# Kernel tuning notes

Measured on AMD Instinct MI355X. Metric: run time of the kernel, lower is better.

Reference implementation:

```python
import jax, jax.numpy as jnp
import numpy as np
from jax.scipy.special import erf, digamma, i0

B, L, D, H = 4, 4096, 512, 4
_MAX_SQRT_GRADIENT = 1000.0

@jax.custom_vjp
def sqrt_bound(x):
    return jnp.sqrt(x)

def _sb_fwd(x):
    return jnp.sqrt(x), x

def _sb_bwd(x, g):
    return (g / jnp.sqrt(jnp.clip(4.0 * x, 1.0 / _MAX_SQRT_GRADIENT**2, None)),)

sqrt_bound.defvjp(_sb_fwd, _sb_bwd)

def block_diag_linear(x, w):
    # x: [..., D], w: [h, bw, bw] block-diagonal weight
    h, bw, _ = w.shape
    xr = x.reshape(x.shape[:-1] + (h, bw))
    return jnp.einsum('...hi,hij->...hj', xr, w).reshape(x.shape)

def self_att_pool(x, num_heads):
    n_state = x.shape[-1] // num_heads
    attn = jax.nn.softmax(jnp.einsum('bld,bmd->blm', x, x) / np.float32(np.sqrt(n_state)), axis=-1)
    # max over the sequence axis of the attended values, keepdims -> [B,1,D]
    return jnp.max(jnp.einsum('blm,bmd->bld', attn, x), axis=-2, keepdims=True)

def ripple_transform_hybrid(t, mix_params):
    mix = jax.nn.softmax(mix_params)
    return mix[0] * digamma(t + 1.0) + mix[1] * i0(t)

def ripple_act(data, alpha, beta, mix_params, temperature=1.0):
    def f(d):
        norm = erf(d / (jnp.max(d) * alpha))
        return jnp.sum(ripple_transform_hybrid(norm * beta, mix_params))
    g = jnp.clip(jax.grad(f)(data), -1.0, 1.0)
    return jax.nn.softmax(-g / temperature, axis=-1)  # softmin

def ripplemoe_act(data, weights, alphas, beta, mix_params, temperature=1.0):
    def f(d):
        dmax = jnp.max(d)
        norm = erf(d[None] / (dmax * alphas[:, None, None]))  # [S,B,L]
        t = ripple_transform_hybrid(norm * beta, mix_params)
        w = jax.nn.softmax(weights)
        return jnp.sum(w[:, None, None] * t)
    g = jnp.clip(jax.grad(f)(data), -1.0, 1.0)
    return jax.nn.softmax(-g / temperature, axis=-1)  # softmin

def token_selection(x, cls_w, cls_b, token_weights, prelu_a, ts_weights, ts_alphas, ts_beta, ts_mix):
    scores = jnp.einsum('bld,sd->sbl', x, cls_w) + cls_b[:, None, None]  # [S,B,L]
    p = jnp.where(scores >= 0, scores, prelu_a * scores)  # PReLU
    ts = jax.nn.celu(p) * jax.nn.silu(p) + jax.nn.gelu(p, approximate=False)
    combined = jnp.einsum('s,sbl->bl', jax.nn.selu(token_weights[:, 0]), ts)
    _, idx = jax.lax.top_k(combined, combined.shape[-1])  # k = L, descending permutation
    vals = ts.sum(0)  # [B,L]
    b_idx = jnp.arange(combined.shape[0])[:, None]
    importance = jnp.ones_like(combined).at[b_idx, idx].add(vals)
    return (1.0 + ripplemoe_act(importance, ts_weights, ts_alphas, ts_beta, ts_mix))[..., None]

def _forward(x, attention_space, W_spatial, W_sil, W_ohead, W_out, w_ig, w_ag, a_param,
             cls_w, cls_b, token_weights, prelu_a, ts_weights, ts_alphas, ts_beta, ts_mix,
             pa1_alpha, pa1_beta, pa1_mix, pa2_alpha, pa2_beta, pa2_mix):
    spatial = jnp.einsum('bld,de->ble', x, attention_space) @ W_spatial.T
    # RG-LRU style gating
    gate_x = jax.nn.sigmoid(block_diag_linear(x, w_ig))
    gate_a = jax.nn.sigmoid(block_diag_linear(x, w_ag))
    log_a = -8.0 * jax.nn.softplus(a_param) * gate_a
    normalized_x = x * gate_x * sqrt_bound(1.0 - jnp.exp(2.0 * log_a))
    gated = jnp.exp(log_a) * self_att_pool(spatial, H) + normalized_x
    sparsity = ripple_act(gated @ W_sil.T, pa1_alpha, pa1_beta, pa1_mix)
    attn = (gated * sparsity) @ W_ohead.T
    sel = token_selection(x, cls_w, cls_b, token_weights, prelu_a, ts_weights, ts_alphas, ts_beta, ts_mix)
    out = ripple_act(attn * sel, pa2_alpha, pa2_beta, pa2_mix)
    return out @ W_out.T

def setup_inputs() -> dict:
    key = jax.random.key(0)
    ks = jax.random.split(key, 12)
    lim = float(1.0 / np.sqrt(D))
    xav = float(np.sqrt(6.0 / (2 * D)))
    bw = D // H
    u = jax.random.uniform(ks[8], (D,), jnp.float32, 0.9**2 + 1e-8, 0.999**2 + 1e-8)
    return {
        'x': jax.random.normal(ks[0], (B, L, D), jnp.float32),
        'attention_space': jax.random.uniform(ks[1], (D, D), jnp.float32, -xav, xav),
        'W_spatial': jax.random.uniform(ks[2], (D, D), jnp.float32, -lim, lim),
        'W_sil': jax.random.uniform(ks[3], (D, D), jnp.float32, -lim, lim),
        'W_ohead': jax.random.uniform(ks[4], (D, D), jnp.float32, -lim, lim),
        'W_out': jax.random.uniform(ks[5], (D, D), jnp.float32, -lim, lim),
        'w_ig': jax.random.normal(ks[6], (H, bw, bw), jnp.float32) * np.float32(np.sqrt(1.0 / bw)),
        'w_ag': jax.random.normal(ks[7], (H, bw, bw), jnp.float32) * np.float32(np.sqrt(1.0 / bw)),
        'a_param': jnp.log(jnp.exp(-0.5 * jnp.log(u)) - 1.0),
        'cls_w': jax.random.uniform(ks[9], (H, D), jnp.float32, -lim, lim),
        'cls_b': jax.random.uniform(ks[10], (H,), jnp.float32, -lim, lim),
        'token_weights': jax.random.normal(ks[11], (H, 1), jnp.float32),
        'prelu_a': jnp.array(0.25, jnp.float32),
        'ts_weights': jnp.ones(H, jnp.float32) / H,
        'ts_alphas': jnp.ones(H, jnp.float32),
        'ts_beta': jnp.array(1.0, jnp.float32),
        'ts_mix': jnp.full((2,), 0.5, jnp.float32),
        'pa1_alpha': jnp.array(1.0, jnp.float32),
        'pa1_beta': jnp.array(1.0, jnp.float32),
        'pa1_mix': jnp.full((2,), 0.5, jnp.float32),
        'pa2_alpha': jnp.array(1.0, jnp.float32),
        'pa2_beta': jnp.array(1.0, jnp.float32),
        'pa2_mix': jnp.full((2,), 0.5, jnp.float32),
    }

def reference(x, attention_space, W_spatial, W_sil, W_ohead, W_out, w_ig, w_ag, a_param,
              cls_w, cls_b, token_weights, prelu_a, ts_weights, ts_alphas, ts_beta, ts_mix,
              pa1_alpha, pa1_beta, pa1_mix, pa2_alpha, pa2_beta, pa2_mix):
    return _forward(x, attention_space, W_spatial, W_sil, W_ohead, W_out, w_ig, w_ag, a_param,
                    cls_w, cls_b, token_weights, prelu_a, ts_weights, ts_alphas, ts_beta, ts_mix,
                    pa1_alpha, pa1_beta, pa1_mix, pa2_alpha, pa2_beta, pa2_mix)
```

## Files before the change

kernel.cpp:

```cpp
#include <hip/hip_runtime.h>

typedef unsigned short ushort;
typedef unsigned int uint;
typedef unsigned long long u64;

#define DEV __device__ __forceinline__

typedef __attribute__((ext_vector_type(4))) float f32x4;
typedef __bf16 bf16x8 __attribute__((ext_vector_type(8)));
typedef __attribute__((ext_vector_type(4))) ushort u16x4;
typedef __attribute__((ext_vector_type(8))) ushort u16x8;

static constexpr int B_ = 4, L_ = 4096, D_ = 512;
static constexpr long NE = (long)B_ * L_ * D_;

DEV float b2f(ushort u) { return __uint_as_float(((uint)u) << 16); }
DEV ushort f2b(float f) {
    uint u = __float_as_uint(f);
    uint r = u + 0x7FFFu + ((u >> 16) & 1u);
    return (ushort)(r >> 16);
}
DEV uint mapF(float f) {
    uint b = __float_as_uint(f);
    return (b & 0x80000000u) ? ~b : (b | 0x80000000u);
}
DEV float unmapF(uint u) {
    uint b = (u & 0x80000000u) ? (u & 0x7FFFFFFFu) : ~u;
    return __uint_as_float(b);
}
DEV float rcp_(float x) { return __builtin_amdgcn_rcpf(x); }
DEV float fexp(float x) { return __builtin_amdgcn_exp2f(x * 1.44269504089f); }
DEV float sigm(float x) { return rcp_(1.f + fexp(-x)); }

DEV void gload16(const ushort* g, ushort* l) {
    __builtin_amdgcn_global_load_lds((const __attribute__((address_space(1))) void*)g,
                                     (__attribute__((address_space(3))) void*)l, 16, 0, 0);
}

DEV int xcd_swz(int b, int nwg) {
    int q = nwg >> 3, r = nwg & 7;
    int x = b & 7, i = b >> 3;
    int base = (x < r) ? x * (q + 1) : r * (q + 1) + (x - r) * q;
    return base + i;
}

DEV float trigamma1p(float t) {
    float x = t + 1.f;
    float acc = 0.f;
#pragma unroll
    for (int k = 0; k < 6; k++) { float xx = x + (float)k; acc += rcp_(xx * xx); }
    float y = x + 6.f;
    float iy = rcp_(y), iy2 = iy * iy;
    return acc + iy * (1.f + iy * (0.5f + iy * (0.166666667f + iy2 * (-0.0333333333f + iy2 * 0.0238095238f))));
}
DEV float besselI1(float t) {
    float q = 0.25f * t * t;
    return 0.5f * t * (1.f + q * (0.5f + q * (0.0833333333f + q * (0.00694444444f + q * (3.47222222e-4f + q * 1.15740741e-5f)))));
}
DEV float rippleH(float u, float beta, float mix0, float mix1) {
    float t = beta * erff(u);
    float Tp = mix0 * trigamma1p(t) + mix1 * besselI1(t);
    float ep = 1.12837917f * fexp(-u * u);
    return beta * Tp * ep;
}

DEV void gemm_core(const ushort* __restrict__ A, int lda,
                   const ushort* __restrict__ Bt, int ldb, int K,
                   ushort* __restrict__ Alds, ushort* __restrict__ Blds,
                   f32x4 (&acc)[4][4])
{
    const int tid = threadIdx.x;
    const int lane = tid & 63;
    const int wave = tid >> 6;
    const int wr = wave >> 1, wc = wave & 1;

    const int srow = wave * 16 + (lane >> 2);
    const int skc = (lane & 3) * 8;
    const ushort* Ag0 = A + (size_t)srow * lda + skc;
    const ushort* Ag1 = A + (size_t)(srow + 64) * lda + skc;
    const ushort* Bg0 = Bt + (size_t)srow * ldb + skc;
    const ushort* Bg1 = Bt + (size_t)(srow + 64) * ldb + skc;
    const int wb = wave * 512;

    const int ar = wr * 64 + (lane & 15);
    const int br = wc * 64 + (lane & 15);
    const int kk = (lane >> 4) * 8;

    gload16(Ag0, Alds + wb);
    gload16(Ag1, Alds + 2048 + wb);
    gload16(Bg0, Blds + wb);
    gload16(Bg1, Blds + 2048 + wb);
    __syncthreads();

    int cur = 0;
    for (int k0 = 0; k0 < K; k0 += 32) {
        const int nb = cur ^ 1;
        if (k0 + 32 < K) {
            gload16(Ag0 + k0 + 32, Alds + nb * 4096 + wb);
            gload16(Ag1 + k0 + 32, Alds + nb * 4096 + 2048 + wb);
            gload16(Bg0 + k0 + 32, Blds + nb * 4096 + wb);
            gload16(Bg1 + k0 + 32, Blds + nb * 4096 + 2048 + wb);
        }
        bf16x8 af[4], bfr[4];
#pragma unroll
        for (int mi = 0; mi < 4; mi++) af[mi] = *(const bf16x8*)&Alds[cur * 4096 + (ar + mi * 16) * 32 + kk];
#pragma unroll
        for (int ni = 0; ni < 4; ni++) bfr[ni] = *(const bf16x8*)&Blds[cur * 4096 + (br + ni * 16) * 32 + kk];
#pragma unroll
        for (int mi = 0; mi < 4; mi++)
#pragma unroll
            for (int ni = 0; ni < 4; ni++)
                acc[mi][ni] = __builtin_amdgcn_mfma_f32_16x16x32_bf16(af[mi], bfr[ni], acc[mi][ni], 0, 0, 0);
        __syncthreads();
        cur = nb;
    }
}

template <int MODE, bool DOMAX>
__global__ __launch_bounds__(256, 2) void gemm_bt(
    const ushort* __restrict__ A, int lda,
    const ushort* __restrict__ Bt, int ldb,
    void* __restrict__ Cv, int ldc, int K,
    const float* __restrict__ rowScale, u64* __restrict__ pmax)
{
    __shared__ ushort Alds[2 * 128 * 32];
    __shared__ ushort Blds[2 * 128 * 32];
    const int nwg = gridDim.x * gridDim.y;
    const int s = xcd_swz(blockIdx.y * gridDim.x + blockIdx.x, nwg);
    const int bx = s % gridDim.x, by = s / gridDim.x;
    const int row0 = by * 128, col0 = bx * 128;
    f32x4 acc[4][4] = {};
    gemm_core(A + (size_t)row0 * lda, lda, Bt + (size_t)col0 * ldb, ldb, K, Alds, Blds, acc);

    const int tid = threadIdx.x;
    const int lane = tid & 63;
    const int wave = tid >> 6;
    const int wr = wave >> 1, wc = wave & 1;
    const int ocol = col0 + wc * 64 + (lane & 15);
    u64 lp = 0;
#pragma unroll
    for (int mi = 0; mi < 4; mi++) {
        const int rbase = row0 + wr * 64 + mi * 16 + (lane >> 4) * 4;
#pragma unroll
        for (int j = 0; j < 4; j++) {
            float sc = (MODE == 3) ? rowScale[rbase + j] : 1.f;
#pragma unroll
            for (int ni = 0; ni < 4; ni++) {
                float v = acc[mi][ni][j] * sc;
                int cc = ocol + ni * 16;
                if (MODE == 1) ((ushort*)Cv)[(size_t)(rbase + j) * ldc + cc] = f2b(v);
                else ((float*)Cv)[(size_t)(rbase + j) * ldc + cc] = v;
                if (DOMAX) {
                    uint idx = (uint)((rbase + j) * ldc + cc);
                    u64 p = ((u64)mapF(v) << 32) | (u64)(~idx);
                    lp = (p > lp) ? p : lp;
                }
            }
        }
    }
    if (DOMAX) {
#pragma unroll
        for (int off = 32; off > 0; off >>= 1) {
            u64 o = __shfl_xor(lp, off);
            lp = (o > lp) ? o : lp;
        }
        if (lane == 0) atomicMax(pmax, lp);
    }
}

__global__ __launch_bounds__(256, 2) void pv_split_k(const ushort* __restrict__ P, const ushort* __restrict__ Vt,
                                                     float* __restrict__ part)
{
    __shared__ ushort Alds[2 * 128 * 32];
    __shared__ ushort Blds[2 * 128 * 32];
    const int ks = blockIdx.z;
    const int nwg = gridDim.x * gridDim.y;
    const int s = xcd_swz(blockIdx.y * gridDim.x + blockIdx.x, nwg);
    const int bx = s % gridDim.x, by = s / gridDim.x;
    const int row0 = by * 128, col0 = bx * 128;
    f32x4 acc[4][4] = {};
    gemm_core(P + (size_t)row0 * 4096 + ks * 1024, 4096,
              Vt + (size_t)col0 * 4096 + ks * 1024, 4096, 1024, Alds, Blds, acc);

    float* C = part + (size_t)ks * 2097152 + (size_t)row0 * 512 + col0;
    const int tid = threadIdx.x;
    const int lane = tid & 63;
    const int wave = tid >> 6;
    const int wr = wave >> 1, wc = wave & 1;
    const int ocol = wc * 64 + (lane & 15);
#pragma unroll
    for (int mi = 0; mi < 4; mi++) {
        const int rl = wr * 64 + mi * 16 + (lane >> 4) * 4;
#pragma unroll
        for (int j = 0; j < 4; j++)
#pragma unroll
            for (int ni = 0; ni < 4; ni++)
                C[(size_t)(rl + j) * 512 + ocol + ni * 16] = acc[mi][ni][j];
    }
}

__global__ __launch_bounds__(256) void pool_combine_k(const float* __restrict__ part, uint* __restrict__ poolU)
{
    const int tid = threadIdx.x;
    const int l0 = blockIdx.x * 32;
    float m0 = -3.4e38f, m1 = -3.4e38f;
    for (int l = 0; l < 32; l++) {
        size_t off = (size_t)(l0 + l) * 512;
        float s0 = 0.f, s1 = 0.f;
#pragma unroll
        for (int ks = 0; ks < 4; ks++) {
            s0 += part[(size_t)ks * 2097152 + off + tid];
            s1 += part[(size_t)ks * 2097152 + off + tid + 256];
        }
        m0 = fmaxf(m0, s0); m1 = fmaxf(m1, s1);
    }
    atomicMax(&poolU[tid], mapF(m0));
    atomicMax(&poolU[tid + 256], mapF(m1));
}

__global__ __launch_bounds__(256, 2) void gate_gemm_k(const ushort* __restrict__ xb,
                                                      const ushort* __restrict__ wigT, const ushort* __restrict__ wagT,
                                                      ushort* __restrict__ gxab, ushort* __restrict__ gaab)
{
    __shared__ ushort Alds[2 * 128 * 32];
    __shared__ ushort Blds[2 * 128 * 32];
    const int which = blockIdx.x;
    const int h = blockIdx.z;
    const ushort* A = xb + (size_t)blockIdx.y * 128 * 512 + h * 128;
    const ushort* W = (which ? wagT : wigT) + (size_t)h * 16384;
    f32x4 acc[4][4] = {};
    gemm_core(A, 512, W, 128, 128, Alds, Blds, acc);

    ushort* C = (which ? gaab : gxab) + (size_t)blockIdx.y * 128 * 512 + h * 128;
    const int tid = threadIdx.x;
    const int lane = tid & 63;
    const int wave = tid >> 6;
    const int wr = wave >> 1, wc = wave & 1;
    const int ocol = wc * 64 + (lane & 15);
#pragma unroll
    for (int mi = 0; mi < 4; mi++) {
        const int rl = wr * 64 + mi * 16 + (lane >> 4) * 4;
#pragma unroll
        for (int j = 0; j < 4; j++)
#pragma unroll
            for (int ni = 0; ni < 4; ni++)
                C[(size_t)(rl + j) * 512 + ocol + ni * 16] = f2b(acc[mi][ni][j]);
    }
}

__global__ void convert_f2b_k(const float* __restrict__ s, ushort* __restrict__ d, long n4) {
    long i = (long)blockIdx.x * blockDim.x + threadIdx.x;
    long st = (long)gridDim.x * blockDim.x;
    for (; i < n4; i += st) {
        f32x4 v = ((const f32x4*)s)[i];
        u16x4 o;
        o[0] = f2b(v[0]); o[1] = f2b(v[1]); o[2] = f2b(v[2]); o[3] = f2b(v[3]);
        ((u16x4*)d)[i] = o;
    }
}

__global__ void convert_w4_k(const float* __restrict__ w0, const float* __restrict__ w1,
                             const float* __restrict__ w2, const float* __restrict__ w3,
                             ushort* __restrict__ dst) {
    const float* srcs[4] = {w0, w1, w2, w3};
    const float* s = srcs[blockIdx.y];
    ushort* d = dst + (size_t)blockIdx.y * 262144;
    int i = blockIdx.x * 256 + threadIdx.x;
    f32x4 v = ((const f32x4*)s)[i];
    u16x4 o;
    o[0] = f2b(v[0]); o[1] = f2b(v[1]); o[2] = f2b(v[2]); o[3] = f2b(v[3]);
    ((u16x4*)d)[i] = o;
}

template <bool SRCF32>
__global__ __launch_bounds__(256) void transpose_to_bf16(const void* __restrict__ srcv, ushort* __restrict__ dst, int R, int C) {
    __shared__ float tile[32][33];
    const int z = blockIdx.z;
    const float* sf = (const float*)srcv + (size_t)z * R * C;
    const ushort* sb = (const ushort*)srcv + (size_t)z * R * C;
    ushort* dz = dst + (size_t)z * R * C;
    const int tx = threadIdx.x & 31, ty = threadIdx.x >> 5;
    const int c = blockIdx.x * 32 + tx;
#pragma unroll
    for (int k = 0; k < 4; k++) {
        const int r = blockIdx.y * 32 + ty + k * 8;
        tile[ty + k * 8][tx] = SRCF32 ? sf[(size_t)r * C + c] : b2f(sb[(size_t)r * C + c]);
    }
    __syncthreads();
#pragma unroll
    for (int k = 0; k < 4; k++) {
        const int dr = blockIdx.x * 32 + ty + k * 8;
        const int dc = blockIdx.y * 32 + tx;
        dz[(size_t)dr * R + dc] = f2b(tile[tx][ty + k * 8]);
    }
}

__global__ __launch_bounds__(256) void transpose_gates_k(const float* __restrict__ wig, const float* __restrict__ wag,
                                                         ushort* __restrict__ wigT, ushort* __restrict__ wagT) {
    __shared__ float tile[32][33];
    const int which = blockIdx.z >> 2, h = blockIdx.z & 3;
    const float* src = (which ? wag : wig) + (size_t)h * 16384;
    ushort* dst = (which ? wagT : wigT) + (size_t)h * 16384;
    const int tx = threadIdx.x & 31, ty = threadIdx.x >> 5;
    const int c = blockIdx.x * 32 + tx;
#pragma unroll
    for (int k = 0; k < 4; k++) {
        const int r = blockIdx.y * 32 + ty + k * 8;
        tile[ty + k * 8][tx] = src[(size_t)r * 128 + c];
    }
    __syncthreads();
#pragma unroll
    for (int k = 0; k < 4; k++) {
        const int dr = blockIdx.x * 32 + ty + k * 8;
        const int dc = blockIdx.y * 32 + tx;
        dst[(size_t)dr * 128 + dc] = f2b(tile[tx][ty + k * 8]);
    }
}

__global__ void init_misc_k(uint* poolU, u64* pmax) {
    int i = blockIdx.x * 256 + threadIdx.x;
    if (i < 2048) poolU[i] = 0u;
    if (i < 4) pmax[i] = 0ull;
}
__global__ void sentinel_k(float* o) { o[threadIdx.x] = 1.0e6f; }

__global__ __launch_bounds__(256) void gates_gated_k(const float* __restrict__ x, const ushort* __restrict__ gxab,
                                                     const ushort* __restrict__ gaab, const float* __restrict__ a_param,
                                                     const uint* __restrict__ poolU, ushort* __restrict__ gatedb) {
    __shared__ float sp8[512];
    const int tid = threadIdx.x;
    for (int d = tid; d < 512; d += 256) {
        float a = a_param[d];
        sp8[d] = 8.f * (fmaxf(a, 0.f) + log1pf(expf(-fabsf(a))));
    }
    __syncthreads();
    long i = (long)blockIdx.x * blockDim.x + tid;
    long st = (long)gridDim.x * blockDim.x;
    const long n8 = NE >> 3;
    for (; i < n8; i += st) {
        u16x8 gx8 = ((const u16x8*)gxab)[i];
        u16x8 ga8 = ((const u16x8*)gaab)[i];
        f32x4 x0 = ((const f32x4*)x)[2 * i];
        f32x4 x1 = ((const f32x4*)x)[2 * i + 1];
        long e = i << 3;
        int b = (int)(e >> 21);
        int d0 = (int)(e & 511);
        u16x8 o;
#pragma unroll
        for (int j = 0; j < 8; j++) {
            float xv = (j < 4) ? x0[j] : x1[j - 4];
            float gx = sigm(b2f(gx8[j]));
            float ga = sigm(b2f(ga8[j]));
            float la = -sp8[d0 + j] * ga;
            float ea = fexp(la);
            float nx = xv * gx * sqrtf(fmaxf(1.f - fexp(2.f * la), 0.f));
            float pl = unmapF(poolU[b * 512 + d0 + j]);
            o[j] = f2b(ea * pl + nx);
        }
        ((u16x8*)gatedb)[i] = o;
    }
}

__global__ __launch_bounds__(256) void softmax_rows_k(const ushort* __restrict__ S, ushort* __restrict__ P, float scale) {
    __shared__ float red[256];
    const int tid = threadIdx.x;
    const ushort* row = S + (size_t)blockIdx.x * 4096;
    float vals[16];
    bf16x8 v0 = *(const bf16x8*)&row[tid * 16];
    bf16x8 v1 = *(const bf16x8*)&row[tid * 16 + 8];
    float mx = -3.4e38f;
#pragma unroll
    for (int k = 0; k < 8; k++) { vals[k] = (float)v0[k] * scale; mx = fmaxf(mx, vals[k]); }
#pragma unroll
    for (int k = 0; k < 8; k++) { vals[8 + k] = (float)v1[k] * scale; mx = fmaxf(mx, vals[8 + k]); }
    red[tid] = mx; __syncthreads();
    for (int s = 128; s > 0; s >>= 1) { if (tid < s) red[tid] = fmaxf(red[tid], red[tid + s]); __syncthreads(); }
    mx = red[0]; __syncthreads();
    float sum = 0.f;
#pragma unroll
    for (int k = 0; k < 16; k++) { vals[k] = fexp(vals[k] - mx); sum += vals[k]; }
    red[tid] = sum; __syncthreads();
    for (int s = 128; s > 0; s >>= 1) { if (tid < s) red[tid] += red[tid + s]; __syncthreads(); }
    float inv = rcp_(red[0]);
    ushort* prow = P + (size_t)blockIdx.x * 4096;
#pragma unroll
    for (int k = 0; k < 16; k++) prow[tid * 16 + k] = f2b(vals[k] * inv);
}

__global__ __launch_bounds__(256) void redmax1_k(const float* __restrict__ d, long n, float* __restrict__ bmax, int* __restrict__ bidx) {
    __shared__ float rv[256];
    __shared__ int ri[256];
    const int tid = threadIdx.x;
    long g = (long)blockIdx.x * 256 + tid;
    const long stride = (long)gridDim.x * 256;
    float bv = -3.4e38f; int bi = -1;
    for (long i = g; i < n; i += stride) {
        float v = d[i];
        if (v > bv) { bv = v; bi = (int)i; }
    }
    rv[tid] = bv; ri[tid] = bi; __syncthreads();
    for (int s = 128; s > 0; s >>= 1) {
        if (tid < s) {
            float ov = rv[tid + s]; int oi = ri[tid + s];
            if (oi >= 0 && (ri[tid] < 0 || ov > rv[tid] || (ov == rv[tid] && oi < ri[tid]))) { rv[tid] = ov; ri[tid] = oi; }
        }
        __syncthreads();
    }
    if (tid == 0) { bmax[blockIdx.x] = rv[0]; bidx[blockIdx.x] = ri[0]; }
}
__global__ __launch_bounds__(256) void redmax2_k(const float* __restrict__ bmax, const int* __restrict__ bidx, int n,
                                                 float* __restrict__ outM, int* __restrict__ outI) {
    __shared__ float rv[256];
    __shared__ int ri[256];
    const int tid = threadIdx.x;
    float bv = -3.4e38f; int bi = -1;
    for (int i = tid; i < n; i += 256) {
        float v = bmax[i]; int ix = bidx[i];
        if (ix >= 0 && (bi < 0 || v > bv || (v == bv && ix < bi))) { bv = v; bi = ix; }
    }
    rv[tid] = bv; ri[tid] = bi; __syncthreads();
    for (int s = 128; s > 0; s >>= 1) {
        if (tid < s) {
            float ov = rv[tid + s]; int oi = ri[tid + s];
            if (oi >= 0 && (ri[tid] < 0 || ov > rv[tid] || (ov == rv[tid] && oi < ri[tid]))) { rv[tid] = ov; ri[tid] = oi; }
        }
        __syncthreads();
    }
    if (tid == 0) { outM[0] = rv[0]; outI[0] = ri[0]; }
}

__global__ __launch_bounds__(256) void ripple_g_k(const float* __restrict__ d, float* __restrict__ gb, float* __restrict__ sspart,
                                                  const u64* __restrict__ pmax, const float* __restrict__ alpha_p,
                                                  const float* __restrict__ beta_p, const float* __restrict__ mix_p) {
    __shared__ float red[256];
    const int tid = threadIdx.x;
    const float M = unmapF((uint)(pmax[0] >> 32));
    const float alpha = alpha_p[0], beta = beta_p[0];
    float m0 = mix_p[0], m1 = mix_p[1];
    float mm = fmaxf(m0, m1);
    float e0 = fexp(m0 - mm), e1 = fexp(m1 - mm);
    float inv = rcp_(e0 + e1);
    float mix0 = e0 * inv, mix1 = e1 * inv;
    const float invMA = rcp_(M * alpha);
    float ss = 0.f;
    long g = (long)blockIdx.x * 256 + tid;
    const long stride = (long)gridDim.x * 256;
    for (long i = g; i < NE; i += stride) {
        float dv = d[i];
        float H = rippleH(dv * invMA, beta, mix0, mix1);
        gb[i] = H * invMA;
        ss += H * dv;
    }
    red[tid] = ss; __syncthreads();
    for (int s = 128; s > 0; s >>= 1) { if (tid < s) red[tid] += red[tid + s]; __syncthreads(); }
    if (tid == 0) sspart[blockIdx.x] = red[0];
}
__global__ __launch_bounds__(256) void redsum2_k(const float* __restrict__ part, int n, float* __restrict__ out) {
    __shared__ float red[256];
    const int tid = threadIdx.x;
    float s = 0.f;
    for (int i = tid; i < n; i += 256) s += part[i];
    red[tid] = s; __syncthreads();
    for (int q = 128; q > 0; q >>= 1) { if (tid < q) red[tid] += red[tid + q]; __syncthreads(); }
    if (tid == 0) out[0] = red[0];
}

template <int GS>
__global__ __launch_bounds__(256) void ripple_softmax_k(const float* __restrict__ gb,
                                                        const u64* __restrict__ pmax,
                                                        const float* __restrict__ ssTot, const float* __restrict__ alpha_p,
                                                        const ushort* __restrict__ gatedb, ushort* __restrict__ outb) {
    __shared__ float red[256];
    const int tid = threadIdx.x;
    const float M = unmapF((uint)(pmax[0] >> 32));
    const int amax = (int)(~(uint)(pmax[0] & 0xFFFFFFFFull));
    const float corr = ssTot[0] * rcp_(M * M * alpha_p[0]);
    long base = (long)blockIdx.x * 512;
    float g0 = gb[base + tid];
    float g1 = gb[base + tid + 256];
    if ((int)(base + tid) == amax) g0 -= corr;
    if ((int)(base + tid + 256) == amax) g1 -= corr;
    g0 = fminf(fmaxf(g0, -1.f), 1.f);
    g1 = fminf(fmaxf(g1, -1.f), 1.f);
    float mn = fminf(g0, g1);
    red[tid] = mn; __syncthreads();
    for (int s = 128; s > 0; s >>= 1) { if (tid < s) red[tid] = fminf(red[tid], red[tid + s]); __syncthreads(); }
    mn = red[0]; __syncthreads();
    float e0 = fexp(mn - g0), e1 = fexp(mn - g1);
    red[tid] = e0 + e1; __syncthreads();
    for (int s = 128; s > 0; s >>= 1) { if (tid < s) red[tid] += red[tid + s]; __syncthreads(); }
    float inv = rcp_(red[0]);
    if (GS) {
        outb[base + tid] = f2b(b2f(gatedb[base + tid]) * (e0 * inv));
        outb[base + tid + 256] = f2b(b2f(gatedb[base + tid + 256]) * (e1 * inv));
    } else {
        outb[base + tid] = f2b(e0 * inv);
        outb[base + tid + 256] = f2b(e1 * inv);
    }
}

__global__ __launch_bounds__(256) void ts1_k(const float* __restrict__ x, const float* __restrict__ cls_w,
                                             const float* __restrict__ cls_b, const float* __restrict__ tw,
                                             const float* __restrict__ prelu_a,
                                             float* __restrict__ combined, float* __restrict__ vals) {
    __shared__ float cw[2048];
    const int tid = threadIdx.x;
    for (int i = tid; i < 2048; i += 256) cw[i] = cls_w[i];
    __syncthreads();
    const int lane = tid & 63, wid = tid >> 6;
    const int row = blockIdx.x * 4 + wid;
    const float* xr = x + (size_t)row * 512 + lane * 8;
    float pa0 = 0, pa1 = 0, pa2 = 0, pa3 = 0;
#pragma unroll
    for (int j = 0; j < 8; j++) {
        float v = xr[j];
        int c = lane * 8 + j;
        pa0 += v * cw[c]; pa1 += v * cw[512 + c]; pa2 += v * cw[1024 + c]; pa3 += v * cw[1536 + c];
    }
#pragma unroll
    for (int o = 32; o > 0; o >>= 1) {
        pa0 += __shfl_down(pa0, o); pa1 += __shfl_down(pa1, o);
        pa2 += __shfl_down(pa2, o); pa3 += __shfl_down(pa3, o);
    }
    if (lane == 0) {
        float a = prelu_a[0];
        float sc[4] = {pa0, pa1, pa2, pa3};
        float comb = 0.f, vsum = 0.f;
#pragma unroll
        for (int s = 0; s < 4; s++) {
            float p = sc[s] + cls_b[s];
            p = (p >= 0.f) ? p : a * p;
            float cel = (p > 0.f) ? p : expm1f(p);
            float sil = p * sigm(p);
            float gel = 0.5f * p * (1.f + erff(p * 0.70710678f));
            float ts = cel * sil + gel;
            float ww = tw[s];
            float se = 1.05070099f * ((ww > 0.f) ? ww : 1.67326324f * expm1f(ww));
            comb += se * ts;
            vsum += ts;
        }
        combined[row] = comb;
        vals[row] = vsum;
    }
}

__global__ __launch_bounds__(256) void ts2a_k(const float* __restrict__ combined, int* __restrict__ rankp) {
    __shared__ float q[512];
    const int b = blockIdx.z;
    const int tid = threadIdx.x;
    const float* cr = combined + b * 4096;
    const int q0 = blockIdx.y * 512;
    for (int i = tid; i < 512; i += 256) q[i] = cr[q0 + i];
    __syncthreads();
    const int p = blockIdx.x * 256 + tid;
    const float cp = cr[p];
    const f32x4* q4 = (const f32x4*)q;
    int rank = 0;
#pragma unroll 8
    for (int i4 = 0; i4 < 128; i4++) {
        f32x4 v = q4[i4];
        int qb = q0 + i4 * 4;
        rank += (v[0] > cp) || (v[0] == cp && (qb + 0) < p);
        rank += (v[1] > cp) || (v[1] == cp && (qb + 1) < p);
        rank += (v[2] > cp) || (v[2] == cp && (qb + 2) < p);
        rank += (v[3] > cp) || (v[3] == cp && (qb + 3) < p);
    }
    rankp[((b * 8 + blockIdx.y) * 4096) + p] = rank;
}

__global__ __launch_bounds__(256) void ts2b_k(const int* __restrict__ rankp, const float* __restrict__ vals,
                                              float* __restrict__ imp) {
    const int b = blockIdx.y;
    const int p = blockIdx.x * 256 + threadIdx.x;
    int rank = 0;
#pragma unroll
    for (int c = 0; c < 8; c++) rank += rankp[((b * 8 + c) * 4096) + p];
    imp[b * 4096 + p] = 1.f + vals[b * 4096 + rank];
}

__global__ __launch_bounds__(256) void moe_g_k(const float* __restrict__ imp, float* __restrict__ gmoe,
                                               float* __restrict__ sspart, const float* __restrict__ scalM,
                                               const float* __restrict__ tsw, const float* __restrict__ tsa,
                                               const float* __restrict__ tsb, const float* __restrict__ tsmix) {
    __shared__ float red[256];
    const int tid = threadIdx.x;
    const float M = scalM[0];
    float w[4], invMA[4], invA[4];
    {
        float wm = fmaxf(fmaxf(tsw[0], tsw[1]), fmaxf(tsw[2], tsw[3]));
        float s = 0.f;
#pragma unroll
        for (int k = 0; k < 4; k++) { w[k] = fexp(tsw[k] - wm); s += w[k]; }
        float si = rcp_(s);
#pragma unroll
        for (int k = 0; k < 4; k++) { w[k] *= si; invMA[k] = rcp_(M * tsa[k]); invA[k] = rcp_(tsa[k]); }
    }
    const float beta = tsb[0];
    float m0 = tsmix[0], m1 = tsmix[1];
    float mm = fmaxf(m0, m1);
    float e0 = fexp(m0 - mm), e1 = fexp(m1 - mm);
    float minv = rcp_(e0 + e1);
    const float mix0 = e0 * minv, mix1 = e1 * minv;

    float ss = 0.f;
    int i = blockIdx.x * 256 + tid;
    const int stride = gridDim.x * 256;
    for (; i < 65536; i += stride) {
        float dv = imp[i];
        float gbv = 0.f;
#pragma unroll
        for (int s = 0; s < 4; s++) {
            float H = rippleH(dv * invMA[s], beta, mix0, mix1);
            gbv += w[s] * H * invMA[s];
            ss += w[s] * H * dv * invA[s];
        }
        gmoe[i] = gbv;
    }
    red[tid] = ss; __syncthreads();
    for (int s = 128; s > 0; s >>= 1) { if (tid < s) red[tid] += red[tid + s]; __syncthreads(); }
    if (tid == 0) sspart[blockIdx.x] = red[0];
}

__global__ __launch_bounds__(256) void moe_sel_k(const float* __restrict__ gmoe, const float* __restrict__ scalM,
                                                 const int* __restrict__ scalI, const float* __restrict__ ssTot,
                                                 float* __restrict__ sel) {
    __shared__ float red[256];
    const int tid = threadIdx.x;
    const int b = blockIdx.x;
    const float M = scalM[0];
    const int amax = scalI[0];
    const float corr = ssTot[0] * rcp_(M * M);
    float g[16];
    float mn = 3.4e38f;
#pragma unroll
    for (int k = 0; k < 16; k++) {
        int i = b * 4096 + tid + k * 256;
        float v = gmoe[i];
        if (i == amax) v -= corr;
        v = fminf(fmaxf(v, -1.f), 1.f);
        g[k] = v;
        mn = fminf(mn, v);
    }
    red[tid] = mn; __syncthreads();
    for (int s = 128; s > 0; s >>= 1) { if (tid < s) red[tid] = fminf(red[tid], red[tid + s]); __syncthreads(); }
    mn = red[0]; __syncthreads();
    float sum = 0.f;
#pragma unroll
    for (int k = 0; k < 16; k++) { g[k] = fexp(mn - g[k]); sum += g[k]; }
    red[tid] = sum; __syncthreads();
    for (int s = 128; s > 0; s >>= 1) { if (tid < s) red[tid] += red[tid + s]; __syncthreads(); }
    float inv = rcp_(red[0]);
#pragma unroll
    for (int k = 0; k < 16; k++) sel[b * 4096 + tid + k * 256] = 1.f + g[k] * inv;
}

static constexpr size_t OFF_XB    = 0;
static constexpr size_t OFF_TMPB  = 16777216;
static constexpr size_t OFF_SPB   = 33554432;
static constexpr size_t OFF_SPT   = 50331648;
static constexpr size_t OFF_DBUF  = 67108864;
static constexpr size_t OFF_HBUF  = 100663296;
static constexpr size_t OFF_GATB  = 134217728;
static constexpr size_t OFF_NXB   = 150994944;
static constexpr size_t OFF_EAB   = 167772160;
static constexpr size_t OFF_AST   = 184549376;
static constexpr size_t OFF_WSP   = 185073664;
static constexpr size_t OFF_WSIL  = 185597952;
static constexpr size_t OFF_WOH   = 186122240;
static constexpr size_t OFF_WOUT  = 186646528;
static constexpr size_t OFF_WIGT  = 187170816;
static constexpr size_t OFF_WAGT  = 187301888;
static constexpr size_t OFF_POOL  = 187432960;
static constexpr size_t OFF_SCAL  = 187441152;
static constexpr size_t OFF_SCALI = 187441408;
static constexpr size_t OFF_BMAX  = 187441664;
static constexpr size_t OFF_BIDX  = 187449856;
static constexpr size_t OFF_SSP   = 187458048;
static constexpr size_t OFF_COMB  = 187466240;
static constexpr size_t OFF_VALS  = 187728384;
static constexpr size_t OFF_IMP   = 187990528;
static constexpr size_t OFF_GMOE  = 188252672;
static constexpr size_t OFF_SEL   = 188514816;
static constexpr size_t WS_NEED   = 188776960;

extern "C" void kernel_launch(void* const* d_in, const int* in_sizes, int n_in,
                              void* d_out, int out_size, void* d_ws, size_t ws_size,
                              hipStream_t stream)
{
    (void)in_sizes; (void)n_in; (void)out_size;
    const float* x    = (const float*)d_in[0];
    const float* AS   = (const float*)d_in[1];
    const float* Wsp  = (const float*)d_in[2];
    const float* Wsil = (const float*)d_in[3];
    const float* Woh  = (const float*)d_in[4];
    const float* Wout = (const float*)d_in[5];
    const float* wig  = (const float*)d_in[6];
    const float* wag  = (const float*)d_in[7];
    const float* a_param = (const float*)d_in[8];
    const float* cls_w = (const float*)d_in[9];
    const float* cls_b = (const float*)d_in[10];
    const float* tokw  = (const float*)d_in[11];
    const float* prelu = (const float*)d_in[12];
    const float* tsw   = (const float*)d_in[13];
    const float* tsa   = (const float*)d_in[14];
    const float* tsb   = (const float*)d_in[15];
    const float* tsmix = (const float*)d_in[16];
    const float* p1a = (const float*)d_in[17];
    const float* p1b = (const float*)d_in[18];
    const float* p1m = (const float*)d_in[19];
    const float* p2a = (const float*)d_in[20];
    const float* p2b = (const float*)d_in[21];
    const float* p2m = (const float*)d_in[22];
    float* out = (float*)d_out;

    char* w = (char*)d_ws;
    if (ws_size < WS_NEED) { sentinel_k<<<1, 256, 0, stream>>>(out); return; }

    ushort* xb    = (ushort*)(w + OFF_XB);
    ushort* tmpb  = (ushort*)(w + OFF_TMPB);
    ushort* spb   = (ushort*)(w + OFF_SPB);
    ushort* spT   = (ushort*)(w + OFF_SPT);
    float*  dbuf  = (float*)(w + OFF_DBUF);
    float*  Hbuf  = (float*)(w + OFF_HBUF);
    ushort* Sb    = (ushort*)(w + OFF_DBUF);
    ushort* Pb    = (ushort*)(w + OFF_HBUF);
    float*  pvpart= (float*)(w + OFF_XB);
    int*    rankp = (int*)(w + OFF_DBUF);
    ushort* gatedb= (ushort*)(w + OFF_GATB);
    ushort* gxab  = (ushort*)(w + OFF_NXB);
    ushort* gaab  = (ushort*)(w + OFF_EAB);
    ushort* ASt   = (ushort*)(w + OFF_AST);
    ushort* Wspb  = (ushort*)(w + OFF_WSP);
    ushort* Wsilb = (ushort*)(w + OFF_WSIL);
    ushort* Wohb  = (ushort*)(w + OFF_WOH);
    ushort* Woutb = (ushort*)(w + OFF_WOUT);
    ushort* wigT  = (ushort*)(w + OFF_WIGT);
    ushort* wagT  = (ushort*)(w + OFF_WAGT);
    uint*   poolU = (uint*)(w + OFF_POOL);
    float*  scal  = (float*)(w + OFF_SCAL);
    u64*    pmax  = (u64*)(w + OFF_SCAL + 128);
    int*    scalI = (int*)(w + OFF_SCALI);
    float*  bmax  = (float*)(w + OFF_BMAX);
    int*    bidx  = (int*)(w + OFF_BIDX);
    float*  sspart= (float*)(w + OFF_SSP);
    float*  comb  = (float*)(w + OFF_COMB);
    float*  vals  = (float*)(w + OFF_VALS);
    float*  imp   = (float*)(w + OFF_IMP);
    float*  gmoe  = (float*)(w + OFF_GMOE);
    float*  sel   = (float*)(w + OFF_SEL);
    ushort* gsb     = tmpb;
    ushort* probs2b = xb;

    convert_f2b_k<<<2048, 256, 0, stream>>>(x, xb, NE >> 2);
    convert_w4_k<<<dim3(256, 4), 256, 0, stream>>>(Wsp, Wsil, Woh, Wout, Wspb);
    transpose_to_bf16<true><<<dim3(16, 16, 1), 256, 0, stream>>>(AS, ASt, 512, 512);
    transpose_gates_k<<<dim3(4, 4, 8), 256, 0, stream>>>(wig, wag, wigT, wagT);
    init_misc_k<<<8, 256, 0, stream>>>(poolU, pmax);

    gate_gemm_k<<<dim3(2, 128, 4), 256, 0, stream>>>(xb, wigT, wagT, gxab, gaab);

    gemm_bt<1, false><<<dim3(4, 128), 256, 0, stream>>>(xb, 512, ASt, 512, tmpb, 512, 512, nullptr, nullptr);
    gemm_bt<1, false><<<dim3(4, 128), 256, 0, stream>>>(tmpb, 512, Wspb, 512, spb, 512, 512, nullptr, nullptr);

    transpose_to_bf16<false><<<dim3(16, 128, 4), 256, 0, stream>>>(spb, spT, 4096, 512);
    const float sc128 = 0.0883883476f;
    for (int b = 0; b < 4; b++) {
        const ushort* spB = spb + (size_t)b * L_ * D_;
        gemm_bt<1, false><<<dim3(32, 32), 256, 0, stream>>>(spB, 512, spB, 512, Sb, 4096, 512, nullptr, nullptr);
        softmax_rows_k<<<4096, 256, 0, stream>>>(Sb, Pb, sc128);
        pv_split_k<<<dim3(4, 32, 4), 256, 0, stream>>>(Pb, spT + (size_t)b * D_ * L_, pvpart);
        pool_combine_k<<<128, 256, 0, stream>>>(pvpart, poolU + b * 512);
    }

    gates_gated_k<<<1024, 256, 0, stream>>>(x, gxab, gaab, a_param, poolU, gatedb);

    gemm_bt<0, true><<<dim3(4, 128), 256, 0, stream>>>(gatedb, 512, Wsilb, 512, dbuf, 512, 512, nullptr, &pmax[0]);
    ripple_g_k<<<2048, 256, 0, stream>>>(dbuf, Hbuf, sspart, &pmax[0], p1a, p1b, p1m);
    redsum2_k<<<1, 256, 0, stream>>>(sspart, 2048, &scal[1]);
    ripple_softmax_k<1><<<16384, 256, 0, stream>>>(Hbuf, &pmax[0], &scal[1], p1a, gatedb, gsb);

    ts1_k<<<4096, 256, 0, stream>>>(x, cls_w, cls_b, tokw, prelu, comb, vals);
    ts2a_k<<<dim3(16, 8, 4), 256, 0, stream>>>(comb, rankp);
    ts2b_k<<<dim3(16, 4), 256, 0, stream>>>(rankp, vals, imp);
    redmax1_k<<<64, 256, 0, stream>>>(imp, 65536, bmax, bidx);
    redmax2_k<<<1, 256, 0, stream>>>(bmax, bidx, 64, &scal[4], &scalI[2]);
    moe_g_k<<<64, 256, 0, stream>>>(imp, gmoe, sspart, &scal[4], tsw, tsa, tsb, tsmix);
    redsum2_k<<<1, 256, 0, stream>>>(sspart, 64, &scal[5]);
    moe_sel_k<<<4, 256, 0, stream>>>(gmoe, &scal[4], &scalI[2], &scal[5], sel);

    gemm_bt<3, true><<<dim3(4, 128), 256, 0, stream>>>(gsb, 512, Wohb, 512, dbuf, 512, 512, sel, &pmax[1]);

    ripple_g_k<<<2048, 256, 0, stream>>>(dbuf, Hbuf, sspart, &pmax[1], p2a, p2b, p2m);
    redsum2_k<<<1, 256, 0, stream>>>(sspart, 2048, &scal[3]);
    ripple_softmax_k<0><<<16384, 256, 0, stream>>>(Hbuf, &pmax[1], &scal[3], p2a, nullptr, probs2b);

    gemm_bt<0, false><<<dim3(4, 128), 256, 0, stream>>>(probs2b, 512, Woutb, 512, out, 512, 512, nullptr, nullptr);
}
```

Baseline: 648.1 us.

## Fuse softmax exponentiation into PV GEMM and defer row normalization

The softmax kernel now writes only the per-row max and reciprocal sum, and the PV GEMM loads raw bf16 scores, exponentiates them in registers and stores the probabilities into LDS itself. Normalization moves into pool_combine as a per-row scale. This removes the write and re-read of the full 4096x4096 bf16 probability matrix per batch. Split-K drops from 4 to 2 and launch bounds rise to 4 waves per SIMD on the GEMMs, which trades register budget for occupancy. The A operand now takes a register-staged load path instead of the direct global-to-LDS load, and the exp work runs inside the main loop.

After: 706.5 us. 1.09x slower.

```diff
diff --git a/kernel.cpp b/kernel.cpp
--- a/kernel.cpp
+++ b/kernel.cpp
@@ -117,7 +117,7 @@
 }
 
 template <int MODE, bool DOMAX>
-__global__ __launch_bounds__(256, 2) void gemm_bt(
+__global__ __launch_bounds__(256, 4) void gemm_bt(
     const ushort* __restrict__ A, int lda,
     const ushort* __restrict__ Bt, int ldb,
     void* __restrict__ Cv, int ldc, int K,
@@ -168,8 +168,8 @@
     }
 }
 
-__global__ __launch_bounds__(256, 2) void pv_split_k(const ushort* __restrict__ P, const ushort* __restrict__ Vt,
-                                                     float* __restrict__ part)
+__global__ __launch_bounds__(256, 4) void pv_fused_k(const ushort* __restrict__ S, const ushort* __restrict__ Vt,
+                                                     const float* __restrict__ mrow, float* __restrict__ part)
 {
     __shared__ ushort Alds[2 * 128 * 32];
     __shared__ ushort Blds[2 * 128 * 32];
@@ -178,15 +178,83 @@
     const int s = xcd_swz(blockIdx.y * gridDim.x + blockIdx.x, nwg);
     const int bx = s % gridDim.x, by = s / gridDim.x;
     const int row0 = by * 128, col0 = bx * 128;
-    f32x4 acc[4][4] = {};
-    gemm_core(P + (size_t)row0 * 4096 + ks * 1024, 4096,
-              Vt + (size_t)col0 * 4096 + ks * 1024, 4096, 1024, Alds, Blds, acc);
-
-    float* C = part + (size_t)ks * 2097152 + (size_t)row0 * 512 + col0;
+    const int koff = ks * 2048;
+    const float sc128 = 0.0883883476f;
+
     const int tid = threadIdx.x;
     const int lane = tid & 63;
     const int wave = tid >> 6;
     const int wr = wave >> 1, wc = wave & 1;
+    const int srow = wave * 16 + (lane >> 2);
+    const int skc = (lane & 3) * 8;
+    const float mr0 = mrow[row0 + srow];
+    const float mr1 = mrow[row0 + srow + 64];
+    const ushort* Ag0 = S + (size_t)(row0 + srow) * 4096 + koff + skc;
+    const ushort* Ag1 = S + (size_t)(row0 + srow + 64) * 4096 + koff + skc;
+    const ushort* Bg0 = Vt + (size_t)(col0 + srow) * 4096 + koff + skc;
+    const ushort* Bg1 = Vt + (size_t)(col0 + srow + 64) * 4096 + koff + skc;
+    const int wb = wave * 512;
+    const int aoff0 = srow * 32 + skc;
+    const int aoff1 = (srow + 64) * 32 + skc;
+
+    const int ar = wr * 64 + (lane & 15);
+    const int br = wc * 64 + (lane & 15);
+    const int kk = (lane >> 4) * 8;
+
+    f32x4 acc[4][4] = {};
+
+    {
+        u16x8 a0 = *(const u16x8*)Ag0;
+        u16x8 a1 = *(const u16x8*)Ag1;
+        gload16(Bg0, Blds + wb);
+        gload16(Bg1, Blds + 2048 + wb);
+        u16x8 p0, p1;
+#pragma unroll
+        for (int j = 0; j < 8; j++) {
+            p0[j] = f2b(fexp(b2f(a0[j]) * sc128 - mr0));
+            p1[j] = f2b(fexp(b2f(a1[j]) * sc128 - mr1));
+        }
+        *(u16x8*)&Alds[aoff0] = p0;
+        *(u16x8*)&Alds[aoff1] = p1;
+    }
+    __syncthreads();
+
+    int cur = 0;
+    for (int k0 = 0; k0 < 2048; k0 += 32) {
+        const int nb = cur ^ 1;
+        const bool more = (k0 + 32) < 2048;
+        u16x8 na0, na1;
+        if (more) {
+            na0 = *(const u16x8*)(Ag0 + k0 + 32);
+            na1 = *(const u16x8*)(Ag1 + k0 + 32);
+            gload16(Bg0 + k0 + 32, Blds + nb * 4096 + wb);
+            gload16(Bg1 + k0 + 32, Blds + nb * 4096 + 2048 + wb);
+        }
+        bf16x8 af[4], bfr[4];
+#pragma unroll
+        for (int mi = 0; mi < 4; mi++) af[mi] = *(const bf16x8*)&Alds[cur * 4096 + (ar + mi * 16) * 32 + kk];
+#pragma unroll
+        for (int ni = 0; ni < 4; ni++) bfr[ni] = *(const bf16x8*)&Blds[cur * 4096 + (br + ni * 16) * 32 + kk];
+#pragma unroll
+        for (int mi = 0; mi < 4; mi++)
+#pragma unroll
+            for (int ni = 0; ni < 4; ni++)
+                acc[mi][ni] = __builtin_amdgcn_mfma_f32_16x16x32_bf16(af[mi], bfr[ni], acc[mi][ni], 0, 0, 0);
+        if (more) {
+            u16x8 p0, p1;
+#pragma unroll
+            for (int j = 0; j < 8; j++) {
+                p0[j] = f2b(fexp(b2f(na0[j]) * sc128 - mr0));
+                p1[j] = f2b(fexp(b2f(na1[j]) * sc128 - mr1));
+            }
+            *(u16x8*)&Alds[nb * 4096 + aoff0] = p0;
+            *(u16x8*)&Alds[nb * 4096 + aoff1] = p1;
+        }
+        __syncthreads();
+        cur = nb;
+    }
+
+    float* C = part + (size_t)ks * 2097152 + (size_t)row0 * 512 + col0;
     const int ocol = wc * 64 + (lane & 15);
 #pragma unroll
     for (int mi = 0; mi < 4; mi++) {
@@ -199,26 +267,24 @@
     }
 }
 
-__global__ __launch_bounds__(256) void pool_combine_k(const float* __restrict__ part, uint* __restrict__ poolU)
+__global__ __launch_bounds__(256) void pool_combine_k(const float* __restrict__ part, const float* __restrict__ invs,
+                                                      uint* __restrict__ poolU)
 {
     const int tid = threadIdx.x;
     const int l0 = blockIdx.x * 32;
     float m0 = -3.4e38f, m1 = -3.4e38f;
     for (int l = 0; l < 32; l++) {
         size_t off = (size_t)(l0 + l) * 512;
-        float s0 = 0.f, s1 = 0.f;
-#pragma unroll
-        for (int ks = 0; ks < 4; ks++) {
-            s0 += part[(size_t)ks * 2097152 + off + tid];
-            s1 += part[(size_t)ks * 2097152 + off + tid + 256];
-        }
+        float iv = invs[l0 + l];
+        float s0 = (part[off + tid] + part[2097152 + off + tid]) * iv;
+        float s1 = (part[off + tid + 256] + part[2097152 + off + tid + 256]) * iv;
         m0 = fmaxf(m0, s0); m1 = fmaxf(m1, s1);
     }
     atomicMax(&poolU[tid], mapF(m0));
     atomicMax(&poolU[tid + 256], mapF(m1));
 }
 
-__global__ __launch_bounds__(256, 2) void gate_gemm_k(const ushort* __restrict__ xb,
+__global__ __launch_bounds__(256, 4) void gate_gemm_k(const ushort* __restrict__ xb,
                                                       const ushort* __restrict__ wigT, const ushort* __restrict__ wagT,
                                                       ushort* __restrict__ gxab, ushort* __restrict__ gaab)
 {
@@ -361,7 +427,8 @@
     }
 }
 
-__global__ __launch_bounds__(256) void softmax_rows_k(const ushort* __restrict__ S, ushort* __restrict__ P, float scale) {
+__global__ __launch_bounds__(256) void softmax_stats_k(const ushort* __restrict__ S, float* __restrict__ mrow,
+                                                       float* __restrict__ invs, float scale) {
     __shared__ float red[256];
     const int tid = threadIdx.x;
     const ushort* row = S + (size_t)blockIdx.x * 4096;
@@ -378,13 +445,10 @@
     mx = red[0]; __syncthreads();
     float sum = 0.f;
 #pragma unroll
-    for (int k = 0; k < 16; k++) { vals[k] = fexp(vals[k] - mx); sum += vals[k]; }
+    for (int k = 0; k < 16; k++) sum += fexp(vals[k] - mx);
     red[tid] = sum; __syncthreads();
     for (int s = 128; s > 0; s >>= 1) { if (tid < s) red[tid] += red[tid + s]; __syncthreads(); }
-    float inv = rcp_(red[0]);
-    ushort* prow = P + (size_t)blockIdx.x * 4096;
-#pragma unroll
-    for (int k = 0; k < 16; k++) prow[tid * 16 + k] = f2b(vals[k] * inv);
+    if (tid == 0) { mrow[blockIdx.x] = mx; invs[blockIdx.x] = rcp_(red[0]); }
 }
 
 __global__ __launch_bounds__(256) void redmax1_k(const float* __restrict__ d, long n, float* __restrict__ bmax, int* __restrict__ bidx) {
@@ -723,7 +787,8 @@
     float*  dbuf  = (float*)(w + OFF_DBUF);
     float*  Hbuf  = (float*)(w + OFF_HBUF);
     ushort* Sb    = (ushort*)(w + OFF_DBUF);
-    ushort* Pb    = (ushort*)(w + OFF_HBUF);
+    float*  mrow  = (float*)(w + OFF_HBUF);
+    float*  invs  = (float*)(w + OFF_HBUF) + 4096;
     float*  pvpart= (float*)(w + OFF_XB);
     int*    rankp = (int*)(w + OFF_DBUF);
     ushort* gatedb= (ushort*)(w + OFF_GATB);
@@ -767,9 +832,9 @@
     for (int b = 0; b < 4; b++) {
         const ushort* spB = spb + (size_t)b * L_ * D_;
         gemm_bt<1, false><<<dim3(32, 32), 256, 0, stream>>>(spB, 512, spB, 512, Sb, 4096, 512, nullptr, nullptr);
-        softmax_rows_k<<<4096, 256, 0, stream>>>(Sb, Pb, sc128);
-        pv_split_k<<<dim3(4, 32, 4), 256, 0, stream>>>(Pb, spT + (size_t)b * D_ * L_, pvpart);
-        pool_combine_k<<<128, 256, 0, stream>>>(pvpart, poolU + b * 512);
+        softmax_stats_k<<<4096, 256, 0, stream>>>(Sb, mrow, invs, sc128);
+        pv_fused_k<<<dim3(4, 32, 2), 256, 0, stream>>>(Sb, spT + (size_t)b * D_ * L_, mrow, pvpart);
+        pool_combine_k<<<128, 256, 0, stream>>>(pvpart, invs, poolU + b * 512);
     }
 
     gates_gated_k<<<1024, 256, 0, stream>>>(x, gxab, gaab, a_param, poolU, gatedb);
```

## Exploit symmetry of x·xᵀ with 256-tile triangular GEMM, batch pairs, in-place softmax

Applied to the files above, without the earlier changes.

Replaces the per-batch 128x128 S=sp·spᵀ GEMM with a 256x256-tile kernel that computes only upper-triangle tiles and writes each off-diagonal tile plus its transpose, processing two batches per launch. The row softmax now runs in place over both batches with vectorized stores. Launch bounds on the other GEMMs are raised to 4 waves per SIMD. This roughly halves the MFMA work and kernel count for the attention scores, at the cost of strided transposed stores and more register pressure in the 512-thread kernel.

Measured after the change: 657.4 us. No clear change (+1.4%).

```diff
diff --git a/kernel.cpp b/kernel.cpp
--- a/kernel.cpp
+++ b/kernel.cpp
@@ -117,7 +117,7 @@
 }
 
 template <int MODE, bool DOMAX>
-__global__ __launch_bounds__(256, 2) void gemm_bt(
+__global__ __launch_bounds__(256, 4) void gemm_bt(
     const ushort* __restrict__ A, int lda,
     const ushort* __restrict__ Bt, int ldb,
     void* __restrict__ Cv, int ldc, int K,
@@ -168,7 +168,97 @@
     }
 }
 
-__global__ __launch_bounds__(256, 2) void pv_split_k(const ushort* __restrict__ P, const ushort* __restrict__ Vt,
+__global__ __launch_bounds__(512, 1) void gemm256_sym_k(
+    const ushort* __restrict__ spP,
+    ushort* __restrict__ Sout)
+{
+    __shared__ ushort Alds[2 * 256 * 32];
+    __shared__ ushort Blds[2 * 256 * 32];
+    const int z = blockIdx.z;
+    int t = xcd_swz(blockIdx.x, 136);
+    int by = 0;
+    while (t >= 16 - by) { t -= 16 - by; by++; }
+    const int bx = by + t;
+    const int row0 = by * 256, col0 = bx * 256;
+    const ushort* A = spP + (size_t)z * (4096 * 512) + (size_t)row0 * 512;
+    const ushort* Bt = spP + (size_t)z * (4096 * 512) + (size_t)col0 * 512;
+
+    const int tid = threadIdx.x;
+    const int lane = tid & 63;
+    const int wave = tid >> 6;
+    const int wr = wave >> 2, wc = wave & 3;
+
+    const int srow = wave * 32 + (lane >> 2);
+    const int skc = (lane & 3) * 8;
+    const ushort* Ag0 = A + (size_t)srow * 512 + skc;
+    const ushort* Ag1 = A + (size_t)(srow + 16) * 512 + skc;
+    const ushort* Bg0 = Bt + (size_t)srow * 512 + skc;
+    const ushort* Bg1 = Bt + (size_t)(srow + 16) * 512 + skc;
+    const int wb = wave * 1024;
+
+    const int ar = wr * 128 + (lane & 15);
+    const int br = wc * 64 + (lane & 15);
+    const int kk = (lane >> 4) * 8;
+
+    f32x4 acc[8][4] = {};
+
+    gload16(Ag0, Alds + wb);
+    gload16(Ag1, Alds + wb + 512);
+    gload16(Bg0, Blds + wb);
+    gload16(Bg1, Blds + wb + 512);
+    __syncthreads();
+
+    int cur = 0;
+    for (int k0 = 0; k0 < 512; k0 += 32) {
+        const int nb = cur ^ 1;
+        if (k0 + 32 < 512) {
+            gload16(Ag0 + k0 + 32, Alds + nb * 8192 + wb);
+            gload16(Ag1 + k0 + 32, Alds + nb * 8192 + wb + 512);
+            gload16(Bg0 + k0 + 32, Blds + nb * 8192 + wb);
+            gload16(Bg1 + k0 + 32, Blds + nb * 8192 + wb + 512);
+        }
+        bf16x8 af[8], bfr[4];
+#pragma unroll
+        for (int mi = 0; mi < 8; mi++) af[mi] = *(const bf16x8*)&Alds[cur * 8192 + (ar + mi * 16) * 32 + kk];
+#pragma unroll
+        for (int ni = 0; ni < 4; ni++) bfr[ni] = *(const bf16x8*)&Blds[cur * 8192 + (br + ni * 16) * 32 + kk];
+#pragma unroll
+        for (int mi = 0; mi < 8; mi++)
+#pragma unroll
+            for (int ni = 0; ni < 4; ni++)
+                acc[mi][ni] = __builtin_amdgcn_mfma_f32_16x16x32_bf16(af[mi], bfr[ni], acc[mi][ni], 0, 0, 0);
+        __syncthreads();
+        cur = nb;
+    }
+
+    ushort* C = Sout + (size_t)z * 16777216;
+    const int ocol = col0 + wc * 64 + (lane & 15);
+#pragma unroll
+    for (int mi = 0; mi < 8; mi++) {
+        const int rbase = row0 + wr * 128 + mi * 16 + (lane >> 4) * 4;
+#pragma unroll
+        for (int j = 0; j < 4; j++)
+#pragma unroll
+            for (int ni = 0; ni < 4; ni++)
+                C[(size_t)(rbase + j) * 4096 + ocol + ni * 16] = f2b(acc[mi][ni][j]);
+    }
+    if (by != bx) {
+#pragma unroll
+        for (int ni = 0; ni < 4; ni++) {
+            const int c = ocol + ni * 16;
+#pragma unroll
+            for (int mi = 0; mi < 8; mi++) {
+                const int r0 = row0 + wr * 128 + mi * 16 + (lane >> 4) * 4;
+                u16x4 v;
+#pragma unroll
+                for (int j = 0; j < 4; j++) v[j] = f2b(acc[mi][ni][j]);
+                *(u16x4*)&C[(size_t)c * 4096 + r0] = v;
+            }
+        }
+    }
+}
+
+__global__ __launch_bounds__(256, 4) void pv_split_k(const ushort* __restrict__ P, const ushort* __restrict__ Vt,
                                                      float* __restrict__ part)
 {
     __shared__ ushort Alds[2 * 128 * 32];
@@ -218,7 +308,7 @@
     atomicMax(&poolU[tid + 256], mapF(m1));
 }
 
-__global__ __launch_bounds__(256, 2) void gate_gemm_k(const ushort* __restrict__ xb,
+__global__ __launch_bounds__(256, 4) void gate_gemm_k(const ushort* __restrict__ xb,
                                                       const ushort* __restrict__ wigT, const ushort* __restrict__ wagT,
                                                       ushort* __restrict__ gxab, ushort* __restrict__ gaab)
 {
@@ -361,10 +451,11 @@
     }
 }
 
-__global__ __launch_bounds__(256) void softmax_rows_k(const ushort* __restrict__ S, ushort* __restrict__ P, float scale) {
+__global__ __launch_bounds__(256) void softmax_rows_k(ushort* __restrict__ Sbase, float scale) {
     __shared__ float red[256];
     const int tid = threadIdx.x;
-    const ushort* row = S + (size_t)blockIdx.x * 4096;
+    const int r = blockIdx.x;
+    ushort* row = Sbase + (size_t)(r >> 12) * 16777216 + (size_t)(r & 4095) * 4096;
     float vals[16];
     bf16x8 v0 = *(const bf16x8*)&row[tid * 16];
     bf16x8 v1 = *(const bf16x8*)&row[tid * 16 + 8];
@@ -382,9 +473,11 @@
     red[tid] = sum; __syncthreads();
     for (int s = 128; s > 0; s >>= 1) { if (tid < s) red[tid] += red[tid + s]; __syncthreads(); }
     float inv = rcp_(red[0]);
-    ushort* prow = P + (size_t)blockIdx.x * 4096;
-#pragma unroll
-    for (int k = 0; k < 16; k++) prow[tid * 16 + k] = f2b(vals[k] * inv);
+    u16x8 o0, o1;
+#pragma unroll
+    for (int k = 0; k < 8; k++) { o0[k] = f2b(vals[k] * inv); o1[k] = f2b(vals[8 + k] * inv); }
+    *(u16x8*)&row[tid * 16] = o0;
+    *(u16x8*)&row[tid * 16 + 8] = o1;
 }
 
 __global__ __launch_bounds__(256) void redmax1_k(const float* __restrict__ d, long n, float* __restrict__ bmax, int* __restrict__ bidx) {
@@ -722,8 +815,7 @@
     ushort* spT   = (ushort*)(w + OFF_SPT);
     float*  dbuf  = (float*)(w + OFF_DBUF);
     float*  Hbuf  = (float*)(w + OFF_HBUF);
-    ushort* Sb    = (ushort*)(w + OFF_DBUF);
-    ushort* Pb    = (ushort*)(w + OFF_HBUF);
+    ushort* Spair = (ushort*)(w + OFF_DBUF);
     float*  pvpart= (float*)(w + OFF_XB);
     int*    rankp = (int*)(w + OFF_DBUF);
     ushort* gatedb= (ushort*)(w + OFF_GATB);
@@ -764,12 +856,16 @@
 
     transpose_to_bf16<false><<<dim3(16, 128, 4), 256, 0, stream>>>(spb, spT, 4096, 512);
     const float sc128 = 0.0883883476f;
-    for (int b = 0; b < 4; b++) {
-        const ushort* spB = spb + (size_t)b * L_ * D_;
-        gemm_bt<1, false><<<dim3(32, 32), 256, 0, stream>>>(spB, 512, spB, 512, Sb, 4096, 512, nullptr, nullptr);
-        softmax_rows_k<<<4096, 256, 0, stream>>>(Sb, Pb, sc128);
-        pv_split_k<<<dim3(4, 32, 4), 256, 0, stream>>>(Pb, spT + (size_t)b * D_ * L_, pvpart);
-        pool_combine_k<<<128, 256, 0, stream>>>(pvpart, poolU + b * 512);
+    for (int p = 0; p < 2; p++) {
+        const ushort* spP = spb + (size_t)(2 * p) * L_ * D_;
+        gemm256_sym_k<<<dim3(136, 1, 2), 512, 0, stream>>>(spP, Spair);
+        softmax_rows_k<<<8192, 256, 0, stream>>>(Spair, sc128);
+        for (int z = 0; z < 2; z++) {
+            const int b = 2 * p + z;
+            pv_split_k<<<dim3(4, 32, 4), 256, 0, stream>>>(Spair + (size_t)z * 16777216,
+                                                           spT + (size_t)b * D_ * L_, pvpart);
+            pool_combine_k<<<128, 256, 0, stream>>>(pvpart, poolU + b * 512);
+        }
     }
 
     gates_gated_k<<<1024, 256, 0, stream>>>(x, gxab, gaab, a_param, poolU, gatedb);
```
